# Kernel optimization log

Measured on AMD Instinct MI355X. Metric: run time of the kernel, lower is better.

The kernel has to match this reference:

```python
import jax, jax.numpy as jnp
import numpy as np

POOL = (32, 32, 32)
P_ENC_DIM = 48
NON_LOCAL_ITER = 2


def _neighbor_graph(spatial):
    # connectivity=2 binary structure in 3x3x3 (k_size=3): 19 offsets with |dx|+|dy|+|dz| <= 2
    D, H, W = spatial
    offs = np.array([(dx, dy, dz) for dx in (-1, 0, 1) for dy in (-1, 0, 1) for dz in (-1, 0, 1)
                     if abs(dx) + abs(dy) + abs(dz) <= 2], dtype=np.int64)  # [K=19,3]
    coords = np.stack(np.meshgrid(np.arange(D), np.arange(H), np.arange(W), indexing='ij'), -1).reshape(-1, 3)
    nbr = coords[:, None, :] + offs[None]                                  # [N,K,3]
    valid = ((nbr >= 0) & (nbr < np.array([D, H, W]))).all(-1)             # [N,K] side nodes lose oob edges
    nbrc = np.clip(nbr, 0, np.array([D - 1, H - 1, W - 1]))
    idx = np.ravel_multi_index(nbrc.reshape(-1, 3).T, (D, H, W)).reshape(valid.shape)
    return jnp.asarray(idx, jnp.int32), jnp.asarray(valid)


def _build_pe(spatial, p_enc_dim, dtype=jnp.float32):
    # sin/cos positional encoding over 3D grid, interleaved per axis (build_geo_feature)
    D, H, W = spatial
    d_model = p_enc_dim // 3
    div = (1e-4) ** (jnp.arange(0, d_model, 2, dtype=dtype) / d_model)     # [d_model//2]
    grids = jnp.meshgrid(jnp.arange(D), jnp.arange(H), jnp.arange(W), indexing='ij')
    parts = []
    for d in range(3):
        ang = grids[d].astype(dtype)[None] * div[:, None, None, None]      # [h,D,H,W]
        parts.append(jnp.stack([jnp.sin(ang), jnp.cos(ang)], 1).reshape(d_model, D, H, W))
    pe = jnp.concatenate(parts, 0)                                         # [p_enc_dim,D,H,W]
    return pe.reshape(p_enc_dim, -1).T                                     # [N,p_enc_dim]


def setup_inputs():
    key = jax.random.key(0)
    ks = jax.random.split(key, 6)
    B, Cf, Cc, FD, GD = 2, 256, 21, 64, 64
    D, H, W = POOL
    neighbor_idx, nbr_mask = _neighbor_graph(POOL)

    def lin(k, fi, fo):
        return jax.random.normal(k, (fi, fo), jnp.float32) / np.sqrt(fi).astype(np.float32)

    return {
        'cam': jax.random.uniform(ks[0], (B, Cc, D, H, W), jnp.float32),
        'f': jax.random.normal(ks[1], (B, Cf, D, H, W), jnp.float32),
        'theta_w': lin(ks[2], Cf, FD), 'theta_b': jnp.zeros((FD,), jnp.float32),
        'phi_w': lin(ks[3], Cf, FD), 'phi_b': jnp.zeros((FD,), jnp.float32),
        'geo_theta_w': lin(ks[4], P_ENC_DIM, GD), 'geo_theta_b': jnp.zeros((GD,), jnp.float32),
        'geo_phi_w': lin(ks[5], P_ENC_DIM, GD), 'geo_phi_b': jnp.zeros((GD,), jnp.float32),
        'neighbor_idx': neighbor_idx, 'nbr_mask': nbr_mask,
    }


def reference(cam, f, theta_w, theta_b, phi_w, phi_b, geo_theta_w, geo_theta_b,
              geo_phi_w, geo_phi_b, neighbor_idx, nbr_mask):
    B, Cc, D, H, W = cam.shape
    N = D * H * W
    f_flat = f.reshape(B, f.shape[1], N).transpose(0, 2, 1)                # [B,N,Cf]
    x_theta = f_flat @ theta_w + theta_b                                    # [B,N,fd]
    x_phi = (f_flat @ phi_w + phi_b)[:, neighbor_idx]                       # [B,N,K,fd] gather
    pe = jax.lax.stop_gradient(_build_pe((D, H, W), P_ENC_DIM, cam.dtype))  # geo feature is detached
    g_theta = pe @ geo_theta_w + geo_theta_b                                # [N,gd]
    g_phi = (pe @ geo_phi_w + geo_phi_b)[neighbor_idx]                      # [N,K,gd]
    # merge_type 'scaled_dot_product_geo': f = theta.phi + geo_theta.geo_phi; softmax(f / sqrt(K))
    scores = jnp.einsum('bnd,bnkd->bnk', x_theta, x_phi) \
           + jnp.einsum('nd,nkd->nk', g_theta, g_phi)[None]
    Kn = scores.shape[-1]
    scores = scores / jnp.sqrt(jnp.asarray(Kn, scores.dtype))
    scores = jnp.where(nbr_mask[None], scores, -jnp.inf)                    # side nodes: fewer edges
    w = jax.nn.softmax(scores, axis=-1)                                     # [B,N,K]
    cam_flat = cam.reshape(B, Cc, N).transpose(0, 2, 1)                     # [B,N,Cc]
    for _ in range(NON_LOCAL_ITER):                                         # weights fixed (f unchanged)
        cam_flat = jnp.einsum('bnk,bnkc->bnc', w, cam_flat[:, neighbor_idx])
    return cam_flat.transpose(0, 2, 1).reshape(B, Cc, D, H, W)
```

## Files before the change

### kernel.cpp

```cpp
#include <hip/hip_runtime.h>
#include <hip/hip_bf16.h>
#include <hip/hip_fp16.h>

#define DD 32
#define HH 32
#define WW 32
#define NN 32768
#define BB 2
#define CF 256
#define CC 21
#define FD 64
#define KK 19

typedef __attribute__((ext_vector_type(8))) short bf16x8;
typedef __attribute__((ext_vector_type(4))) float f32x4;

__device__ const int OFF[19][3] = {
    {-1,-1, 0}, {-1, 0,-1}, {-1, 0, 0}, {-1, 0, 1}, {-1, 1, 0},
    { 0,-1,-1}, { 0,-1, 0}, { 0,-1, 1}, { 0, 0,-1}, { 0, 0, 0},
    { 0, 0, 1}, { 0, 1,-1}, { 0, 1, 0}, { 0, 1, 1},
    { 1,-1, 0}, { 1, 0,-1}, { 1, 0, 0}, { 1, 0, 1}, { 1, 1, 0}
};

__device__ __forceinline__ unsigned short f2bf(float x) {
    unsigned u = __float_as_uint(x);
    u += 0x7FFFu + ((u >> 16) & 1u);
    return (unsigned short)(u >> 16);
}
__device__ __forceinline__ float bf2f(unsigned short h) {
    return __uint_as_float((unsigned)h << 16);
}
#define QF(x) (((x) & 3) ^ (((x) >> 2) & 3))

__global__ __launch_bounds__(256) void tbl_kernel(
    const float* __restrict__ gtw, const float* __restrict__ gtb,
    const float* __restrict__ gpw, const float* __restrict__ gpb,
    const float* __restrict__ thw, const float* __restrict__ phw,
    float* __restrict__ Tg, uint4* __restrict__ whi, uint4* __restrict__ wlo)
{
    int blk = blockIdx.x, tid = threadIdx.x;
    if (blk >= 10) {
        int gid = (blk - 10) * 256 + tid;
        int col = gid & 127;
        int kb = (gid >> 7) & 3;
        int ks = gid >> 9;
        const float* src = (col < 64) ? (thw + col) : (phw + (col - 64));
        int kbase = ks * 32 + kb * 8;
        unsigned hi4[4], lo4[4];
#pragma unroll
        for (int e2 = 0; e2 < 4; ++e2) {
            float va = src[(kbase + 2 * e2) * 64];
            float vb = src[(kbase + 2 * e2 + 1) * 64];
            unsigned short ha = f2bf(va), hb = f2bf(vb);
            unsigned short la = f2bf(va - bf2f(ha)), lb = f2bf(vb - bf2f(hb));
            hi4[e2] = (unsigned)ha | ((unsigned)hb << 16);
            lo4[e2] = (unsigned)la | ((unsigned)lb << 16);
        }
        int idx = (ks * 4 + kb) * 128 + col;
        whi[idx] = make_uint4(hi4[0], hi4[1], hi4[2], hi4[3]);
        wlo[idx] = make_uint4(lo4[0], lo4[1], lo4[2], lo4[3]);
        return;
    }

    __shared__ float pe_s[32][16];
    for (int i = tid; i < 512; i += 256) {
        int c = i >> 4, q = i & 15;
        int ii = q >> 1;
        float div = expf(-9.210340371976184f * (float)ii * 0.125f);
        float ang = (float)c * div;
        pe_s[c][q] = (q & 1) ? cosf(ang) : sinf(ang);
    }
    __syncthreads();

    __shared__ float panels[6][32][65];
    int npan = (blk == 9) ? 6 : 2;
#pragma unroll 1
    for (int pp = 0; pp < npan; ++pp) {
        int axis, isP;
        if (blk == 9) { axis = pp % 3; isP = pp / 3; }
        else          { axis = (pp == 0) ? (blk / 3) : (blk % 3); isP = pp; }
        const float* W = isP ? gpw : gtw;
#pragma unroll
        for (int e = 0; e < 8; ++e) {
            int idx = e * 256 + tid;
            int c = idx >> 6, j = idx & 63;
            float acc = 0.f;
#pragma unroll
            for (int q = 0; q < 16; ++q)
                acc = fmaf(pe_s[c][q], W[(axis * 16 + q) * 64 + j], acc);
            panels[pp][c][j] = acc;
        }
    }
    __syncthreads();

    if (blk < 9) {
        bool tr = (blk == 6) || (blk == 7);
#pragma unroll
        for (int e = 0; e < 4; ++e) {
            int idx = e * 256 + tid;
            int x = idx >> 5, y = idx & 31;
            float s = 0.f;
#pragma unroll
            for (int j = 0; j < 64; ++j)
                s = fmaf(panels[0][x][j], panels[1][y][j], s);
            Tg[blk * 1024 + (tr ? (y * 32 + x) : (x * 32 + y))] = s;
        }
    } else {
        if (tid < 96) {
            int ax = tid >> 5, c = tid & 31;
            float s = 0.f;
#pragma unroll
            for (int j = 0; j < 64; ++j) s = fmaf(panels[ax][c][j], gpb[j], s);
            Tg[9216 + ax * 32 + c] = s;
        } else if (tid < 192) {
            int t2 = tid - 96;
            int ax = t2 >> 5, c = t2 & 31;
            float s = 0.f;
#pragma unroll
            for (int j = 0; j < 64; ++j) s = fmaf(gtb[j], panels[3 + ax][c][j], s);
            Tg[9312 + ax * 32 + c] = s;
        } else if (tid == 192) {
            float s = 0.f;
#pragma unroll
            for (int j = 0; j < 64; ++j) s = fmaf(gtb[j], gpb[j], s);
            Tg[9408] = s;
        }
    }
}

__global__ __launch_bounds__(256) void proj_kernel(
    const float* __restrict__ f,
    const uint4* __restrict__ whi, const uint4* __restrict__ wlo,
    const float* __restrict__ thb, const float* __restrict__ phb,
    float* __restrict__ theta, __half* __restrict__ phi)
{
    __shared__ __align__(16) unsigned short Ahi[128][4][8];
    __shared__ __align__(16) unsigned short Alo[128][4][8];
    __shared__ __align__(16) unsigned short Bhi[128][4][8];
    __shared__ __align__(16) unsigned short Blo[128][4][8];

    int tid = threadIdx.x;
    int b = blockIdx.x >> 8;
    int n0 = (blockIdx.x & 255) * 128;
    int wv = tid >> 6, lane = tid & 63;
    int wr = (wv >> 1) * 64, wc = (wv & 1) * 64;
    int fr = lane & 15, kb_r = lane >> 4;

    int srow = tid & 127;
    int kb0 = (tid >> 7) * 2;

    const float* fb = f + (size_t)b * CF * NN + n0;

    f32x4 acc[4][4];
#pragma unroll
    for (int mi = 0; mi < 4; ++mi)
#pragma unroll
        for (int ni = 0; ni < 4; ++ni) acc[mi][ni] = (f32x4){0.f, 0.f, 0.f, 0.f};

#pragma unroll 1
    for (int k0 = 0; k0 < CF; k0 += 32) {
#pragma unroll
        for (int i = 0; i < 2; ++i) {
            int kb = kb0 + i;
            const float* src = fb + (size_t)(k0 + kb * 8) * NN + srow;
            unsigned hi4[4], lo4[4];
#pragma unroll
            for (int e2 = 0; e2 < 4; ++e2) {
                float va = src[(size_t)(2 * e2) * NN];
                float vb = src[(size_t)(2 * e2 + 1) * NN];
                unsigned short ha = f2bf(va), hb = f2bf(vb);
                unsigned short la = f2bf(va - bf2f(ha)), lb = f2bf(vb - bf2f(hb));
                hi4[e2] = (unsigned)ha | ((unsigned)hb << 16);
                lo4[e2] = (unsigned)la | ((unsigned)lb << 16);
            }
            int slot = kb ^ QF(srow);
            *(uint4*)&Ahi[srow][slot][0] = make_uint4(hi4[0], hi4[1], hi4[2], hi4[3]);
            *(uint4*)&Alo[srow][slot][0] = make_uint4(lo4[0], lo4[1], lo4[2], lo4[3]);
        }
        {
            const uint4* wh = whi + (size_t)(k0 >> 5) * 4 * 128;
            const uint4* wl = wlo + (size_t)(k0 >> 5) * 4 * 128;
#pragma unroll
            for (int i = 0; i < 2; ++i) {
                int kb = kb0 + i;
                uint4 hh = wh[kb * 128 + srow];
                uint4 ll = wl[kb * 128 + srow];
                int slot = kb ^ QF(srow);
                *(uint4*)&Bhi[srow][slot][0] = hh;
                *(uint4*)&Blo[srow][slot][0] = ll;
            }
        }
        __syncthreads();
        bf16x8 ah[4], al[4], bh[4], bl[4];
#pragma unroll
        for (int mi = 0; mi < 4; ++mi) {
            int r = wr + mi * 16 + fr;
            int slot = kb_r ^ QF(r);
            ah[mi] = *(const bf16x8*)&Ahi[r][slot][0];
            al[mi] = *(const bf16x8*)&Alo[r][slot][0];
        }
#pragma unroll
        for (int ni = 0; ni < 4; ++ni) {
            int c = wc + ni * 16 + fr;
            int slot = kb_r ^ QF(c);
            bh[ni] = *(const bf16x8*)&Bhi[c][slot][0];
            bl[ni] = *(const bf16x8*)&Blo[c][slot][0];
        }
#pragma unroll
        for (int mi = 0; mi < 4; ++mi)
#pragma unroll
            for (int ni = 0; ni < 4; ++ni) {
                acc[mi][ni] = __builtin_amdgcn_mfma_f32_16x16x32_bf16(ah[mi], bh[ni], acc[mi][ni], 0, 0, 0);
                acc[mi][ni] = __builtin_amdgcn_mfma_f32_16x16x32_bf16(al[mi], bh[ni], acc[mi][ni], 0, 0, 0);
                acc[mi][ni] = __builtin_amdgcn_mfma_f32_16x16x32_bf16(ah[mi], bl[ni], acc[mi][ni], 0, 0, 0);
            }
        __syncthreads();
    }

#pragma unroll
    for (int ni = 0; ni < 4; ++ni) {
        int j = wc + ni * 16 + fr;
        if (j < 64) {
            float bj = thb[j];
            float* outp = theta + (size_t)b * NN * 64 + j;
#pragma unroll
            for (int mi = 0; mi < 4; ++mi) {
                int nbase = n0 + wr + mi * 16 + kb_r * 4;
#pragma unroll
                for (int r = 0; r < 4; ++r)
                    outp[(size_t)(nbase + r) * 64] = acc[mi][ni][r] + bj;
            }
        } else {
            float bj = phb[j - 64];
            __half* outp = phi + (size_t)b * NN * 64 + (j - 64);
#pragma unroll
            for (int mi = 0; mi < 4; ++mi) {
                int nbase = n0 + wr + mi * 16 + kb_r * 4;
#pragma unroll
                for (int r = 0; r < 4; ++r)
                    outp[(size_t)(nbase + r) * 64] = __float2half(acc[mi][ni][r] + bj);
            }
        }
    }
}

__global__ __launch_bounds__(256) void gsc_kernel(
    const float* __restrict__ Tg, float* __restrict__ gsc)
{
    __shared__ float Ts[9 * 1024];
    __shared__ float UVs[193];
    int tid = threadIdx.x;
#pragma unroll
    for (int i = 0; i < 9; ++i) {
        int idx = i * 1024 + tid;
        Ts[idx] = Tg[idx];
        Ts[idx + 256] = Tg[idx + 256];
        Ts[idx + 512] = Tg[idx + 512];
        Ts[idx + 768] = Tg[idx + 768];
    }
    if (tid < 193) UVs[tid] = Tg[9216 + tid];
    __syncthreads();

    int n = blockIdx.x * 256 + tid;
    int d = n >> 10, h = (n >> 5) & 31, w = n & 31;
    float Un = UVs[d] + UVs[32 + h] + UVs[64 + w] + UVs[192];
    const float rs = 0.2294157338705618f;

#pragma unroll
    for (int k = 0; k < KK; ++k) {
        int nd = d + OFF[k][0], nh = h + OFF[k][1], nw = w + OFF[k][2];
        bool valid = ((unsigned)nd < 32u) && ((unsigned)nh < 32u) && ((unsigned)nw < 32u);
        int ndc = min(max(nd, 0), 31), nhc = min(max(nh, 0), 31), nwc = min(max(nw, 0), 31);
        float g = Ts[0 * 1024 + d * 32 + ndc] + Ts[1 * 1024 + d * 32 + nhc]
                + Ts[2 * 1024 + d * 32 + nwc] + Ts[3 * 1024 + h * 32 + ndc]
                + Ts[4 * 1024 + h * 32 + nhc] + Ts[5 * 1024 + h * 32 + nwc]
                + Ts[6 * 1024 + ndc * 32 + w] + Ts[7 * 1024 + nhc * 32 + w]
                + Ts[8 * 1024 + w * 32 + nwc]
                + Un + UVs[96 + ndc] + UVs[128 + nhc] + UVs[160 + nwc];
        gsc[(size_t)k * NN + n] = valid ? g * rs : -INFINITY;
    }
}

__global__ __launch_bounds__(256) void score_kernel(
    const float* __restrict__ theta, const __half* __restrict__ phi,
    const float* __restrict__ gsc, float* __restrict__ wgt)
{
    int tid = threadIdx.x;
    int lane = tid & 63;
    int wv = tid >> 6;
    int sub = lane >> 4;
    int col4 = lane & 15;
    int gn = blockIdx.x * 16 + wv * 4 + sub;
    int b = gn >> 15;
    int n = gn & (NN - 1);
    int d = n >> 10, h = (n >> 5) & 31, w = n & 31;

    float4 tq = *(const float4*)(theta + (size_t)gn * 64 + col4 * 4);
    const __half* pb = phi + (size_t)b * NN * 64;
    const float* gr = gsc + n;
    const float rs = 0.2294157338705618f;

    float s[KK];
#pragma unroll
    for (int k = 0; k < KK; ++k) {
        int nd = d + OFF[k][0], nh = h + OFF[k][1], nw = w + OFF[k][2];
        nd = min(max(nd, 0), 31); nh = min(max(nh, 0), 31); nw = min(max(nw, 0), 31);
        int nn = (nd << 10) + (nh << 5) + nw;
        uint2 raw = *(const uint2*)(pb + (size_t)nn * 64 + col4 * 4);
        __half2 h01 = __builtin_bit_cast(__half2, raw.x);
        __half2 h23 = __builtin_bit_cast(__half2, raw.y);
        float2 f01 = __half22float2(h01), f23 = __half22float2(h23);
        float part = tq.x * f01.x + tq.y * f01.y + tq.z * f23.x + tq.w * f23.y;
        part += __shfl_xor(part, 1, 16);
        part += __shfl_xor(part, 2, 16);
        part += __shfl_xor(part, 4, 16);
        part += __shfl_xor(part, 8, 16);
        s[k] = fmaf(part, rs, gr[(size_t)k * NN]);
    }
    float m = s[0];
#pragma unroll
    for (int k = 1; k < KK; ++k) m = fmaxf(m, s[k]);
    float sum = 0.f;
#pragma unroll
    for (int k = 0; k < KK; ++k) { s[k] = __expf(s[k] - m); sum += s[k]; }
    float inv = 1.f / sum;
#pragma unroll
    for (int kk2 = 0; kk2 < 2; ++kk2) {
        int k = kk2 * 16 + col4;
        if (k < KK) wgt[((size_t)b * KK + k) * NN + n] = s[k] * inv;
    }
}

__global__ __launch_bounds__(256) void prop_kernel(
    const float* __restrict__ cin, const float* __restrict__ wgt,
    float* __restrict__ cout)
{
    int gid = blockIdx.x * 256 + threadIdx.x;
    int n = gid & (NN - 1);
    int rest = gid >> 15;
    int b = rest / 3, cg = rest % 3;
    int c0 = cg * 7;
    int d = n >> 10, h = (n >> 5) & 31, w = n & 31;

    const float* wb = wgt + (size_t)b * KK * NN + n;
    int nidx[KK];
    float wv[KK];
#pragma unroll
    for (int k = 0; k < KK; ++k) {
        int nd = d + OFF[k][0], nh = h + OFF[k][1], nw = w + OFF[k][2];
        nd = min(max(nd, 0), 31); nh = min(max(nh, 0), 31); nw = min(max(nw, 0), 31);
        nidx[k] = (nd << 10) + (nh << 5) + nw;
        wv[k] = wb[(size_t)k * NN];
    }

    const float* cb = cin + ((size_t)b * CC + c0) * NN;
    float* co = cout + ((size_t)b * CC + c0) * NN + n;
#pragma unroll
    for (int cc = 0; cc < 7; ++cc) {
        float acc = 0.f;
#pragma unroll
        for (int k = 0; k < KK; ++k)
            acc = fmaf(wv[k], cb[nidx[k]], acc);
        co[(size_t)cc * NN] = acc;
        cb += NN;
    }
}

extern "C" void kernel_launch(void* const* d_in, const int* in_sizes, int n_in,
                              void* d_out, int out_size, void* d_ws, size_t ws_size,
                              hipStream_t stream) {
    const float* cam = (const float*)d_in[0];
    const float* f   = (const float*)d_in[1];
    const float* thw = (const float*)d_in[2];
    const float* thb = (const float*)d_in[3];
    const float* phw = (const float*)d_in[4];
    const float* phb = (const float*)d_in[5];
    const float* gtw = (const float*)d_in[6];
    const float* gtb = (const float*)d_in[7];
    const float* gpw = (const float*)d_in[8];
    const float* gpb = (const float*)d_in[9];

    float*  ws    = (float*)d_ws;
    float*  theta = ws;
    __half* phi   = (__half*)(theta + (size_t)BB * NN * 64);
    float*  wgt   = (float*)((char*)phi + (size_t)BB * NN * 64 * 2);
    float*  gsc   = wgt + (size_t)BB * KK * NN;
    float*  cam1  = gsc + (size_t)KK * NN;
    uint4*  whi   = (uint4*)(cam1 + (size_t)BB * CC * NN);
    uint4*  wlo   = whi + 4096;
    float*  Tg    = (float*)(wlo + 4096);

    tbl_kernel<<<26, 256, 0, stream>>>(gtw, gtb, gpw, gpb, thw, phw, Tg, whi, wlo);
    proj_kernel<<<512, 256, 0, stream>>>(f, whi, wlo, thb, phb, theta, phi);
    gsc_kernel<<<NN / 256, 256, 0, stream>>>(Tg, gsc);
    score_kernel<<<BB * NN / 16, 256, 0, stream>>>(theta, phi, gsc, wgt);
    prop_kernel<<<BB * NN * 3 / 256, 256, 0, stream>>>(cam, wgt, cam1);
    prop_kernel<<<BB * NN * 3 / 256, 256, 0, stream>>>(cam1, wgt, (float*)d_out);
}
```

Baseline: 72.88 us.

## Store theta as fp16 and double K-step per sync in projection GEMM

Theta, previously stored as fp32, is now written as fp16 like phi, and score_kernel reads and converts it. This halves theta's write and read traffic at some cost in precision. The projection GEMM now stages 64 input channels per iteration instead of 32 and runs two MFMA sub-steps per barrier pair. The LDS swizzle and the weight table layout are adjusted to the new 8-slot layout. Each block uses more shared memory, which may reduce occupancy.

```diff
diff --git a/kernel.cpp b/kernel.cpp
--- a/kernel.cpp
+++ b/kernel.cpp
@@ -30,7 +30,6 @@
 __device__ __forceinline__ float bf2f(unsigned short h) {
     return __uint_as_float((unsigned)h << 16);
 }
-#define QF(x) (((x) & 3) ^ (((x) >> 2) & 3))
 
 __global__ __launch_bounds__(256) void tbl_kernel(
     const float* __restrict__ gtw, const float* __restrict__ gtb,
@@ -42,10 +41,9 @@
     if (blk >= 10) {
         int gid = (blk - 10) * 256 + tid;
         int col = gid & 127;
-        int kb = (gid >> 7) & 3;
-        int ks = gid >> 9;
+        int g8 = gid >> 7;
         const float* src = (col < 64) ? (thw + col) : (phw + (col - 64));
-        int kbase = ks * 32 + kb * 8;
+        int kbase = g8 * 8;
         unsigned hi4[4], lo4[4];
 #pragma unroll
         for (int e2 = 0; e2 < 4; ++e2) {
@@ -56,7 +54,7 @@
             hi4[e2] = (unsigned)ha | ((unsigned)hb << 16);
             lo4[e2] = (unsigned)la | ((unsigned)lb << 16);
         }
-        int idx = (ks * 4 + kb) * 128 + col;
+        int idx = g8 * 128 + col;
         whi[idx] = make_uint4(hi4[0], hi4[1], hi4[2], hi4[3]);
         wlo[idx] = make_uint4(lo4[0], lo4[1], lo4[2], lo4[3]);
         return;
@@ -132,12 +130,12 @@
     const float* __restrict__ f,
     const uint4* __restrict__ whi, const uint4* __restrict__ wlo,
     const float* __restrict__ thb, const float* __restrict__ phb,
-    float* __restrict__ theta, __half* __restrict__ phi)
-{
-    __shared__ __align__(16) unsigned short Ahi[128][4][8];
-    __shared__ __align__(16) unsigned short Alo[128][4][8];
-    __shared__ __align__(16) unsigned short Bhi[128][4][8];
-    __shared__ __align__(16) unsigned short Blo[128][4][8];
+    __half* __restrict__ theta, __half* __restrict__ phi)
+{
+    __shared__ __align__(16) unsigned short Ahi[128][8][8];
+    __shared__ __align__(16) unsigned short Alo[128][8][8];
+    __shared__ __align__(16) unsigned short Bhi[128][8][8];
+    __shared__ __align__(16) unsigned short Blo[128][8][8];
 
     int tid = threadIdx.x;
     int b = blockIdx.x >> 8;
@@ -147,7 +145,7 @@
     int fr = lane & 15, kb_r = lane >> 4;
 
     int srow = tid & 127;
-    int kb0 = (tid >> 7) * 2;
+    int kb0 = (tid >> 7) * 4;
 
     const float* fb = f + (size_t)b * CF * NN + n0;
 
@@ -158,9 +156,9 @@
         for (int ni = 0; ni < 4; ++ni) acc[mi][ni] = (f32x4){0.f, 0.f, 0.f, 0.f};
 
 #pragma unroll 1
-    for (int k0 = 0; k0 < CF; k0 += 32) {
-#pragma unroll
-        for (int i = 0; i < 2; ++i) {
+    for (int k0 = 0; k0 < CF; k0 += 64) {
+#pragma unroll
+        for (int i = 0; i < 4; ++i) {
             int kb = kb0 + i;
             const float* src = fb + (size_t)(k0 + kb * 8) * NN + srow;
             unsigned hi4[4], lo4[4];
@@ -173,73 +171,66 @@
                 hi4[e2] = (unsigned)ha | ((unsigned)hb << 16);
                 lo4[e2] = (unsigned)la | ((unsigned)lb << 16);
             }
-            int slot = kb ^ QF(srow);
+            int slot = kb ^ (srow & 7);
             *(uint4*)&Ahi[srow][slot][0] = make_uint4(hi4[0], hi4[1], hi4[2], hi4[3]);
             *(uint4*)&Alo[srow][slot][0] = make_uint4(lo4[0], lo4[1], lo4[2], lo4[3]);
         }
         {
-            const uint4* wh = whi + (size_t)(k0 >> 5) * 4 * 128;
-            const uint4* wl = wlo + (size_t)(k0 >> 5) * 4 * 128;
-#pragma unroll
-            for (int i = 0; i < 2; ++i) {
+            const uint4* wh = whi + (size_t)(k0 >> 3) * 128;
+            const uint4* wl = wlo + (size_t)(k0 >> 3) * 128;
+#pragma unroll
+            for (int i = 0; i < 4; ++i) {
                 int kb = kb0 + i;
                 uint4 hh = wh[kb * 128 + srow];
                 uint4 ll = wl[kb * 128 + srow];
-                int slot = kb ^ QF(srow);
+                int slot = kb ^ (srow & 7);
                 *(uint4*)&Bhi[srow][slot][0] = hh;
                 *(uint4*)&Blo[srow][slot][0] = ll;
             }
         }
         __syncthreads();
-        bf16x8 ah[4], al[4], bh[4], bl[4];
-#pragma unroll
-        for (int mi = 0; mi < 4; ++mi) {
-            int r = wr + mi * 16 + fr;
-            int slot = kb_r ^ QF(r);
-            ah[mi] = *(const bf16x8*)&Ahi[r][slot][0];
-            al[mi] = *(const bf16x8*)&Alo[r][slot][0];
-        }
-#pragma unroll
-        for (int ni = 0; ni < 4; ++ni) {
-            int c = wc + ni * 16 + fr;
-            int slot = kb_r ^ QF(c);
-            bh[ni] = *(const bf16x8*)&Bhi[c][slot][0];
-            bl[ni] = *(const bf16x8*)&Blo[c][slot][0];
-        }
-#pragma unroll
-        for (int mi = 0; mi < 4; ++mi)
+#pragma unroll
+        for (int c = 0; c < 2; ++c) {
+            bf16x8 ah[4], al[4], bh[4], bl[4];
+            int kb_c = c * 4 + kb_r;
+#pragma unroll
+            for (int mi = 0; mi < 4; ++mi) {
+                int r = wr + mi * 16 + fr;
+                int slot = kb_c ^ (r & 7);
+                ah[mi] = *(const bf16x8*)&Ahi[r][slot][0];
+                al[mi] = *(const bf16x8*)&Alo[r][slot][0];
+            }
 #pragma unroll
             for (int ni = 0; ni < 4; ++ni) {
-                acc[mi][ni] = __builtin_amdgcn_mfma_f32_16x16x32_bf16(ah[mi], bh[ni], acc[mi][ni], 0, 0, 0);
-                acc[mi][ni] = __builtin_amdgcn_mfma_f32_16x16x32_bf16(al[mi], bh[ni], acc[mi][ni], 0, 0, 0);
-                acc[mi][ni] = __builtin_amdgcn_mfma_f32_16x16x32_bf16(ah[mi], bl[ni], acc[mi][ni], 0, 0, 0);
+                int col = wc + ni * 16 + fr;
+                int slot = kb_c ^ (col & 7);
+                bh[ni] = *(const bf16x8*)&Bhi[col][slot][0];
+                bl[ni] = *(const bf16x8*)&Blo[col][slot][0];
             }
+#pragma unroll
+            for (int mi = 0; mi < 4; ++mi)
+#pragma unroll
+                for (int ni = 0; ni < 4; ++ni) {
+                    acc[mi][ni] = __builtin_amdgcn_mfma_f32_16x16x32_bf16(ah[mi], bh[ni], acc[mi][ni], 0, 0, 0);
+                    acc[mi][ni] = __builtin_amdgcn_mfma_f32_16x16x32_bf16(al[mi], bh[ni], acc[mi][ni], 0, 0, 0);
+                    acc[mi][ni] = __builtin_amdgcn_mfma_f32_16x16x32_bf16(ah[mi], bl[ni], acc[mi][ni], 0, 0, 0);
+                }
+        }
         __syncthreads();
     }
 
 #pragma unroll
     for (int ni = 0; ni < 4; ++ni) {
         int j = wc + ni * 16 + fr;
-        if (j < 64) {
-            float bj = thb[j];
-            float* outp = theta + (size_t)b * NN * 64 + j;
-#pragma unroll
-            for (int mi = 0; mi < 4; ++mi) {
-                int nbase = n0 + wr + mi * 16 + kb_r * 4;
-#pragma unroll
-                for (int r = 0; r < 4; ++r)
-                    outp[(size_t)(nbase + r) * 64] = acc[mi][ni][r] + bj;
-            }
-        } else {
-            float bj = phb[j - 64];
-            __half* outp = phi + (size_t)b * NN * 64 + (j - 64);
-#pragma unroll
-            for (int mi = 0; mi < 4; ++mi) {
-                int nbase = n0 + wr + mi * 16 + kb_r * 4;
-#pragma unroll
-                for (int r = 0; r < 4; ++r)
-                    outp[(size_t)(nbase + r) * 64] = __float2half(acc[mi][ni][r] + bj);
-            }
+        float bj = (j < 64) ? thb[j] : phb[j - 64];
+        __half* outp = (j < 64) ? (theta + (size_t)b * NN * 64 + j)
+                                : (phi + (size_t)b * NN * 64 + (j - 64));
+#pragma unroll
+        for (int mi = 0; mi < 4; ++mi) {
+            int nbase = n0 + wr + mi * 16 + kb_r * 4;
+#pragma unroll
+            for (int r = 0; r < 4; ++r)
+                outp[(size_t)(nbase + r) * 64] = __float2half(acc[mi][ni][r] + bj);
         }
     }
 }
@@ -282,7 +273,7 @@
 }
 
 __global__ __launch_bounds__(256) void score_kernel(
-    const float* __restrict__ theta, const __half* __restrict__ phi,
+    const __half* __restrict__ theta, const __half* __restrict__ phi,
     const float* __restrict__ gsc, float* __restrict__ wgt)
 {
     int tid = threadIdx.x;
@@ -295,7 +286,12 @@
     int n = gn & (NN - 1);
     int d = n >> 10, h = (n >> 5) & 31, w = n & 31;
 
-    float4 tq = *(const float4*)(theta + (size_t)gn * 64 + col4 * 4);
+    uint2 traw = *(const uint2*)(theta + (size_t)gn * 64 + col4 * 4);
+    __half2 t01 = __builtin_bit_cast(__half2, traw.x);
+    __half2 t23 = __builtin_bit_cast(__half2, traw.y);
+    float2 tf01 = __half22float2(t01), tf23 = __half22float2(t23);
+    float4 tq = {tf01.x, tf01.y, tf23.x, tf23.y};
+
     const __half* pb = phi + (size_t)b * NN * 64;
     const float* gr = gsc + n;
     const float rs = 0.2294157338705618f;
@@ -381,9 +377,9 @@
     const float* gpb = (const float*)d_in[9];
 
     float*  ws    = (float*)d_ws;
-    float*  theta = ws;
-    __half* phi   = (__half*)(theta + (size_t)BB * NN * 64);
-    float*  wgt   = (float*)((char*)phi + (size_t)BB * NN * 64 * 2);
+    __half* theta = (__half*)ws;
+    __half* phi   = theta + (size_t)BB * NN * 64;
+    float*  wgt   = (float*)(phi + (size_t)BB * NN * 64);
     float*  gsc   = wgt + (size_t)BB * KK * NN;
     float*  cam1  = gsc + (size_t)KK * NN;
     uint4*  whi   = (uint4*)(cam1 + (size_t)BB * CC * NN);
```

Result: no change. 71.72 us (-1.6%).
